# Kernel tuning notes

Hardware: AMD Instinct MI355X
Metric: run time of the kernel (lower is better)

The kernel has to match this reference:

```python
import jax, jax.numpy as jnp
import numpy as np

B, H, W = 8, 1024, 1024

SOBEL_X = jnp.array([[-1, 0, 1], [-2, 0, 2], [-1, 0, 1]], jnp.float32).reshape(1, 1, 3, 3)
SOBEL_Y = jnp.array([[-1, -2, -1], [0, 0, 0], [1, 2, 1]], jnp.float32).reshape(1, 1, 3, 3)
LAPLACIAN = jnp.array([[0, -1, 0], [-1, 4, -1], [0, -1, 0]], jnp.float32).reshape(1, 1, 3, 3)
TWO_PI = 2.0 * np.pi


def _conv(x, k, pad):
    return jax.lax.conv_general_dilated(
        x, k, window_strides=(1, 1), padding=[(pad, pad), (pad, pad)],
        dimension_numbers=('NCHW', 'OIHW', 'NCHW'))


def _boundary_mask(mask, w):
    ks = 2 * w + 1
    kernel = jnp.ones((1, 1, ks, ks), jnp.float32)
    s = _conv(mask, kernel, w)
    dilated = (s > 0).astype(jnp.float32)
    eroded = (s >= float(ks * ks)).astype(jnp.float32)
    return jnp.clip(dilated - eroded, 0.0, 1.0)


def _elev_grads(e):
    gx = _conv(e, SOBEL_X, 1)
    gy = _conv(e, SOBEL_Y, 1)
    mag = jnp.sqrt(gx * gx + gy * gy + 1e-8)
    dirn = jnp.arctan2(gy, gx + 1e-8)
    curv = _conv(e, LAPLACIAN, 1)
    return mag, dirn, curv


def _high_freq_mask(h, w):
    ii, jj = jnp.meshgrid(jnp.arange(h, dtype=jnp.float32), jnp.arange(w, dtype=jnp.float32), indexing='ij')
    dist = jnp.sqrt((ii - h // 2) ** 2 + (jj - w // 2) ** 2)
    return (dist > min(h, w) * 0.3).astype(jnp.float32).reshape(1, 1, h, w)


def setup_inputs() -> dict:
    key = jax.random.key(0)
    k1, k2, k3 = jax.random.split(key, 3)
    pred = jax.random.normal(k1, (B, 1, H, W), jnp.float32)
    target = jax.random.normal(k2, (B, 1, H, W), jnp.float32)
    mask = jax.random.randint(k3, (B, 1, H, W), 0, 2).astype(jnp.float32)
    return {'pred_elevation': pred, 'target_elevation': target, 'mask': mask}


def reference(pred_elevation, target_elevation, mask):
    # boundary masks for widths 1..3
    bms = [_boundary_mask(mask, w) for w in (1, 2, 3)]

    # ---- gradient continuity loss ----
    p_mag, p_dir, p_curv = _elev_grads(pred_elevation)
    t_mag, t_dir, t_curv = _elev_grads(target_elevation)
    slope_diff = jnp.abs(p_mag - t_mag)
    dir_diff = jnp.abs(p_dir - t_dir)
    dir_diff = jnp.minimum(dir_diff, TWO_PI - dir_diff)
    curv_diff = jnp.abs(p_curv - t_curv)
    grad_loss = 0.0
    for i, bm in enumerate(bms):
        w_sd = 1.0 if i == 0 else 0.5
        w_cv = 2.0 if i == 0 else 1.0
        grad_loss = grad_loss + w_sd * jnp.mean(slope_diff * bm)
        grad_loss = grad_loss + w_sd * jnp.mean(dir_diff * bm)
        grad_loss = grad_loss + w_cv * jnp.mean(curv_diff * bm)
    grad_loss = grad_loss / len(bms)

    # ---- frequency continuity loss ----
    pf = jnp.fft.fft2(pred_elevation)
    tf = jnp.fft.fft2(target_elevation)
    p_magf, t_magf = jnp.abs(pf), jnp.abs(tf)
    p_ph = jnp.arctan2(pf.imag, pf.real)
    t_ph = jnp.arctan2(tf.imag, tf.real)
    hf = _high_freq_mask(H, W)
    mag_loss = jnp.mean((p_magf * hf - t_magf * hf) ** 2)
    d = p_ph - t_ph
    phase_diff = jnp.arctan2(jnp.sin(d), jnp.cos(d))  # wrap to (-pi, pi]
    phase_loss = jnp.mean((phase_diff * hf) ** 2)
    freq_loss = mag_loss + 2.0 * phase_loss

    # ---- smoothness constraint (width_1 only) ----
    kern9 = jnp.ones((1, 1, 3, 3), jnp.float32) / 9.0
    local_mean = _conv(pred_elevation, kern9, 1)
    local_mean_sq = _conv(pred_elevation ** 2, kern9, 1)
    local_var = jnp.clip(local_mean_sq - local_mean ** 2, 1e-8, None)
    local_std = jnp.sqrt(local_var)
    smooth_loss = jnp.mean(local_std * bms[0])

    # ---- slope continuity (width_1 only) ----
    psx = _conv(p_mag, SOBEL_X, 1)
    psy = _conv(p_mag, SOBEL_Y, 1)
    p_change = jnp.sqrt(psx ** 2 + psy ** 2 + 1e-8)
    tsx = _conv(t_mag, SOBEL_X, 1)
    tsy = _conv(t_mag, SOBEL_Y, 1)
    t_change = jnp.sqrt(tsx ** 2 + tsy ** 2 + 1e-8)
    slope_loss = jnp.mean(jnp.abs(p_change - t_change) * bms[0])

    total = 2.0 * grad_loss + 1.5 * freq_loss + 3.0 * smooth_loss + 2.0 * slope_loss
    return (total, grad_loss, freq_loss, smooth_loss, slope_loss)
```

## Files before the change

### kernel.cpp

```cpp
#include <hip/hip_runtime.h>

#define HW 1024
#define TWO_PI_F 6.28318530717958647692f
#define NSLOT 64

__device__ __forceinline__ float2 cmulf(float2 a, float2 b){
  return make_float2(a.x*b.x - a.y*b.y, a.x*b.y + a.y*b.x);
}
__device__ __forceinline__ float fsqrt(float x){ return __builtin_amdgcn_sqrtf(x); }

__device__ __forceinline__ float fast_atan2_abs(float ay, float x){
  float ax = fabsf(x);
  float mx = fmaxf(ax, ay), mn = fminf(ax, ay);
  float a  = mn * __builtin_amdgcn_rcpf(fmaxf(mx, 1e-37f));
  float s  = a * a;
  float r  = ((((0.0208351f*s - 0.085133f)*s + 0.180141f)*s - 0.3302995f)*s
              + 0.999866f) * a;
  r = (ay > ax) ? 1.57079632679f - r : r;
  return (x < 0.f) ? 3.14159265359f - r : r;
}

__device__ __forceinline__ float block_reduce_add_f(float v, float* sc){
  int tid = threadIdx.x;
  #pragma unroll
  for (int o = 32; o > 0; o >>= 1) v += __shfl_down(v, o, 64);
  __syncthreads();
  if ((tid & 63) == 0) sc[tid >> 6] = v;
  __syncthreads();
  return sc[0] + sc[1] + sc[2] + sc[3];
}

__global__ void setup_kernel(double* acc, float2* twg){
  int i = threadIdx.x + blockIdx.x * 256;
  if (i < 5 * NSLOT) acc[i] = 0.0;
  if (i < 512){
    float s, c; sincosf(-TWO_PI_F * (float)i * (1.f/1024.f), &s, &c);
    twg[i] = make_float2(c, s);
  }
}

__global__ __launch_bounds__(256)
void spatial_kernel(const float* __restrict__ pred, const float* __restrict__ targ,
                    const float* __restrict__ mask, double* __restrict__ acc){
  __shared__ float sp[36*44];
  __shared__ float st[36*44];
  __shared__ float ov[2*34*35];
  __shared__ unsigned long long mrow[38];
  __shared__ float sc[4];
  float* const smkf = ov;
  float* const pmg  = ov;
  float* const tmg  = ov + 34*35;

  const int tid = threadIdx.x;
  const int x0 = blockIdx.x << 5, y0 = blockIdx.y << 5;
  const int z = blockIdx.z;
  const size_t ib = (size_t)z * ((size_t)HW * HW);
  const bool interior = ((unsigned)(blockIdx.x - 1) < 30u) &&
                        ((unsigned)(blockIdx.y - 1) < 30u);

  if (interior){
    const float* pb = pred + ib;
    const float* tb = targ + ib;
    for (int i = tid; i < 360; i += 256){
      int a = i / 10, b = i % 10;
      size_t off = (size_t)(y0 - 2 + a) * HW + (x0 - 4 + 4*b);
      float4 pv = *(const float4*)(pb + off);
      float4 tv = *(const float4*)(tb + off);
      int o = a*44 + 4*b;
      sp[o]=pv.x; sp[o+1]=pv.y; sp[o+2]=pv.z; sp[o+3]=pv.w;
      st[o]=tv.x; st[o+1]=tv.y; st[o+2]=tv.z; st[o+3]=tv.w;
    }
    const float* mb = mask + ib;
    for (int i = tid; i < 380; i += 256){
      int a = i / 10, b = i % 10;
      size_t off = (size_t)(y0 - 3 + a) * HW + (x0 - 4 + 4*b);
      float4 v = *(const float4*)(mb + off);
      int o = a*41 + 4*b;
      smkf[o]=v.x; smkf[o+1]=v.y; smkf[o+2]=v.z; smkf[o+3]=v.w;
    }
  } else {
    for (int i = tid; i < 1296; i += 256){
      int a = i / 36, b = i % 36;
      int gy = y0 - 2 + a, gx = x0 - 2 + b;
      float pv = 0.f, tv = 0.f;
      if ((unsigned)gy < HW && (unsigned)gx < HW){
        size_t idx = ib + (size_t)gy * HW + gx;
        pv = pred[idx]; tv = targ[idx];
      }
      sp[a*44 + b + 2] = pv; st[a*44 + b + 2] = tv;
    }
    for (int i = tid; i < 1444; i += 256){
      int a = i / 38, b = i % 38;
      int gy = y0 - 3 + a, gx = x0 - 3 + b;
      float v = 0.f;
      if ((unsigned)gy < HW && (unsigned)gx < HW) v = mask[ib + (size_t)gy * HW + gx];
      smkf[a*41 + b + 1] = v;
    }
  }
  __syncthreads();

  if (tid < 38){
    unsigned long long w = 0ull;
    #pragma unroll
    for (int x = 0; x < 38; x++)
      w |= (smkf[tid*41 + 1 + x] > 0.5f) ? (1ull << x) : 0ull;
    mrow[tid] = w;
  }
  __syncthreads();

  for (int i = tid; i < 1156; i += 256){
    int iy = i / 34, ix = i % 34;
    int gy = y0 - 1 + iy, gx = x0 - 1 + ix;
    float pv = 0.f, tv = 0.f;
    if ((unsigned)gy < HW && (unsigned)gx < HW){
      int o = iy*44 + ix + 2;
      float a00=sp[o], a01=sp[o+1], a02=sp[o+2];
      float a10=sp[o+44],           a12=sp[o+46];
      float a20=sp[o+88], a21=sp[o+89], a22=sp[o+90];
      float gxp = (a02 + 2.f*a12 + a22) - (a00 + 2.f*a10 + a20);
      float gyp = (a20 + 2.f*a21 + a22) - (a00 + 2.f*a01 + a02);
      pv = fsqrt(gxp*gxp + gyp*gyp + 1e-8f);
      float b00=st[o], b01=st[o+1], b02=st[o+2];
      float b10=st[o+44],           b12=st[o+46];
      float b20=st[o+88], b21=st[o+89], b22=st[o+90];
      float gxt = (b02 + 2.f*b12 + b22) - (b00 + 2.f*b10 + b20);
      float gyt = (b20 + 2.f*b21 + b22) - (b00 + 2.f*b01 + b02);
      tv = fsqrt(gxt*gxt + gyt*gyt + 1e-8f);
    }
    pmg[iy*35+ix] = pv; tmg[iy*35+ix] = tv;
  }
  __syncthreads();

  const int ty = tid >> 5, tx = tid & 31;
  const int r0 = ty << 2;

  int c1[10], c2[10], c3[10];
  #pragma unroll
  for (int j = 0; j < 10; j++){
    unsigned w = (unsigned)(mrow[r0 + j] >> tx);
    c3[j] = __popc(w & 0x7Fu);
    c2[j] = __popc((w >> 1) & 0x1Fu);
    c1[j] = __popc((w >> 2) & 0x7u);
  }

  float P[3][3], Q[3][3], A[3][3], B[3][3];
  #pragma unroll
  for (int rr = 0; rr < 3; rr++)
    #pragma unroll
    for (int cc = 0; cc < 3; cc++){
      P[rr][cc] = sp[(r0+1+rr)*44 + tx+3+cc];
      Q[rr][cc] = st[(r0+1+rr)*44 + tx+3+cc];
      A[rr][cc] = pmg[(r0+rr)*35 + tx+cc];
      B[rr][cc] = tmg[(r0+rr)*35 + tx+cc];
    }

  float accg = 0.f, accs = 0.f, accl = 0.f;
  #pragma unroll
  for (int k = 0; k < 4; k++){
    if (k){
      #pragma unroll
      for (int cc = 0; cc < 3; cc++){
        P[0][cc]=P[1][cc]; P[1][cc]=P[2][cc]; P[2][cc]=sp[(r0+k+3)*44 + tx+3+cc];
        Q[0][cc]=Q[1][cc]; Q[1][cc]=Q[2][cc]; Q[2][cc]=st[(r0+k+3)*44 + tx+3+cc];
        A[0][cc]=A[1][cc]; A[1][cc]=A[2][cc]; A[2][cc]=pmg[(r0+k+2)*35 + tx+cc];
        B[0][cc]=B[1][cc]; B[1][cc]=B[2][cc]; B[2][cc]=tmg[(r0+k+2)*35 + tx+cc];
      }
    }
    float gxp = (P[0][2]+2.f*P[1][2]+P[2][2]) - (P[0][0]+2.f*P[1][0]+P[2][0]);
    float gyp = (P[2][0]+2.f*P[2][1]+P[2][2]) - (P[0][0]+2.f*P[0][1]+P[0][2]);
    float cvp = 4.f*P[1][1] - P[0][1] - P[1][0] - P[1][2] - P[2][1];
    float gxt = (Q[0][2]+2.f*Q[1][2]+Q[2][2]) - (Q[0][0]+2.f*Q[1][0]+Q[2][0]);
    float gyt = (Q[2][0]+2.f*Q[2][1]+Q[2][2]) - (Q[0][0]+2.f*Q[0][1]+Q[0][2]);
    float cvt = 4.f*Q[1][1] - Q[0][1] - Q[1][0] - Q[1][2] - Q[2][1];

    float sd = fabsf(A[1][1] - B[1][1]);
    float x1 = gxp + 1e-8f, y1 = gyp;
    float x2 = gxt + 1e-8f, y2 = gyt;
    float dd = fast_atan2_abs(fabsf(y1*x2 - x1*y2), x1*x2 + y1*y2);
    float cd = fabsf(cvp - cvt);

    int s1 = c1[k+2]+c1[k+3]+c1[k+4];
    int s2 = c2[k+1]+c2[k+2]+c2[k+3]+c2[k+4]+c2[k+5];
    int s3 = c3[k]+c3[k+1]+c3[k+2]+c3[k+3]+c3[k+4]+c3[k+5]+c3[k+6];
    float w1 = ((unsigned)(s1 - 1) <  8u) ? 1.f : 0.f;
    float w2 = ((unsigned)(s2 - 1) < 24u) ? 1.f : 0.f;
    float w3 = ((unsigned)(s3 - 1) < 48u) ? 1.f : 0.f;

    accg += (sd + dd) * (w1 + 0.5f*(w2 + w3)) + cd * (2.f*w1 + w2 + w3);

    float s9 = 0.f, s9q = 0.f;
    #pragma unroll
    for (int rr = 0; rr < 3; rr++)
      #pragma unroll
      for (int cc = 0; cc < 3; cc++){ s9 += P[rr][cc]; s9q += P[rr][cc]*P[rr][cc]; }
    float lm = s9 * (1.f/9.f), lq = s9q * (1.f/9.f);
    accs += fsqrt(fmaxf(lq - lm*lm, 1e-8f)) * w1;

    float psx = (A[0][2]+2.f*A[1][2]+A[2][2]) - (A[0][0]+2.f*A[1][0]+A[2][0]);
    float psy = (A[2][0]+2.f*A[2][1]+A[2][2]) - (A[0][0]+2.f*A[0][1]+A[0][2]);
    float pch = fsqrt(psx*psx + psy*psy + 1e-8f);
    float tsx = (B[0][2]+2.f*B[1][2]+B[2][2]) - (B[0][0]+2.f*B[1][0]+B[2][0]);
    float tsy = (B[2][0]+2.f*B[2][1]+B[2][2]) - (B[0][0]+2.f*B[0][1]+B[0][2]);
    float tch = fsqrt(tsx*tsx + tsy*tsy + 1e-8f);
    accl += fabsf(pch - tch) * w1;
  }

  float g  = block_reduce_add_f(accg, sc);
  float sm = block_reduce_add_f(accs, sc);
  float sl = block_reduce_add_f(accl, sc);
  if (tid == 0){
    int slot = (blockIdx.x + blockIdx.y * 7 + z * 13) & (NSLOT - 1);
    atomicAdd(&acc[0*NSLOT + slot], (double)g);
    atomicAdd(&acc[1*NSLOT + slot], (double)sm);
    atomicAdd(&acc[2*NSLOT + slot], (double)sl);
  }
}

__device__ __forceinline__ float lane_xor(float x, int h, int lane){
  int xi = __float_as_int(x);
  int r;
  if (h == 1)       r = __builtin_amdgcn_update_dpp(xi, xi, 0xB1, 0xF, 0xF, true);
  else if (h == 2)  r = __builtin_amdgcn_update_dpp(xi, xi, 0x4E, 0xF, 0xF, true);
  else if (h == 8)  r = __builtin_amdgcn_update_dpp(xi, xi, 0x128, 0xF, 0xF, true);
  else if (h == 4)  r = __builtin_amdgcn_ds_swizzle(xi, 0x101F);
  else if (h == 16) r = __builtin_amdgcn_ds_swizzle(xi, 0x401F);
  else              r = __builtin_amdgcn_ds_bpermute((lane ^ 32) << 2, xi);
  return __int_as_float(r);
}

#define FC 0.70710678118654752f
#define FC1 0.92387953251128676f
#define FS1 0.38268343236508977f

__device__ __forceinline__ void bfly(float2& a, float2& b){
  float tx = b.x, ty = b.y;
  b.x = a.x - tx; b.y = a.y - ty;
  a.x += tx;      a.y += ty;
}
__device__ __forceinline__ void cmul_c(float2& b, float wr, float wi){
  float tx = wr*b.x - wi*b.y, ty = wr*b.y + wi*b.x;
  b.x = tx; b.y = ty;
}
__device__ __forceinline__ void rotmi(float2& b){
  float t = b.x; b.x = b.y; b.y = -t;
}

__device__ __forceinline__ void fft16_reg(float2* v){
  float2 y[16];
  y[0]=v[0];  y[1]=v[8];  y[2]=v[4];  y[3]=v[12];
  y[4]=v[2];  y[5]=v[10]; y[6]=v[6];  y[7]=v[14];
  y[8]=v[1];  y[9]=v[9];  y[10]=v[5]; y[11]=v[13];
  y[12]=v[3]; y[13]=v[11];y[14]=v[7]; y[15]=v[15];
  #pragma unroll
  for (int g = 0; g < 8; g++) bfly(y[2*g], y[2*g+1]);
  #pragma unroll
  for (int g = 0; g < 4; g++){
    int b = 4*g;
    bfly(y[b], y[b+2]);
    rotmi(y[b+3]); bfly(y[b+1], y[b+3]);
  }
  #pragma unroll
  for (int g = 0; g < 2; g++){
    int b = 8*g;
    bfly(y[b], y[b+4]);
    cmul_c(y[b+5],  FC, -FC); bfly(y[b+1], y[b+5]);
    rotmi(y[b+6]);            bfly(y[b+2], y[b+6]);
    cmul_c(y[b+7], -FC, -FC); bfly(y[b+3], y[b+7]);
  }
  bfly(y[0], y[8]);
  cmul_c(y[9],   FC1, -FS1); bfly(y[1], y[9]);
  cmul_c(y[10],  FC,  -FC);  bfly(y[2], y[10]);
  cmul_c(y[11],  FS1, -FC1); bfly(y[3], y[11]);
  rotmi(y[12]);              bfly(y[4], y[12]);
  cmul_c(y[13], -FS1, -FC1); bfly(y[5], y[13]);
  cmul_c(y[14], -FC,  -FC);  bfly(y[6], y[14]);
  cmul_c(y[15], -FC1, -FS1); bfly(y[7], y[15]);
  #pragma unroll
  for (int j = 0; j < 16; j++) v[j] = y[j];
}

__device__ __forceinline__ void fft1024_wave(float2* v, int lane,
                                             const float2* __restrict__ twg){
  {
    const float sgn = (lane & 1) ? -1.f : 1.f;
    #pragma unroll
    for (int j = 0; j < 16; j++){
      float ox = lane_xor(v[j].x, 1, lane);
      float oy = lane_xor(v[j].y, 1, lane);
      v[j].x = fmaf(sgn, v[j].x, ox);
      v[j].y = fmaf(sgn, v[j].y, oy);
    }
  }
  #pragma unroll
  for (int s = 1; s < 6; s++){
    const int h = 1 << s;
    const bool up = (lane & h) != 0;
    const float2 w = twg[(lane & (h - 1)) << (9 - s)];
    const float ewx = up ? w.x : 1.f;
    const float ewy = up ? w.y : 0.f;
    const float sgn = up ? -1.f : 1.f;
    #pragma unroll
    for (int j = 0; j < 16; j++){
      float tx = ewx*v[j].x - ewy*v[j].y;
      float ty = ewx*v[j].y + ewy*v[j].x;
      float ox = lane_xor(tx, h, lane);
      float oy = lane_xor(ty, h, lane);
      v[j].x = fmaf(sgn, tx, ox);
      v[j].y = fmaf(sgn, ty, oy);
    }
  }
  float2 w1 = twg[lane];
  float2 w2 = cmulf(w1, w1);
  float2 w3 = cmulf(w2, w1);
  float2 w4 = cmulf(w2, w2);
  float2 w5 = cmulf(w3, w2);
  float2 w6 = cmulf(w3, w3);
  float2 w7 = cmulf(w4, w3);
  float2 w8 = cmulf(w4, w4);
  v[1]  = cmulf(v[1],  w1);
  v[2]  = cmulf(v[2],  w2);
  v[3]  = cmulf(v[3],  w3);
  v[4]  = cmulf(v[4],  w4);
  v[5]  = cmulf(v[5],  w5);
  v[6]  = cmulf(v[6],  w6);
  v[7]  = cmulf(v[7],  w7);
  v[8]  = cmulf(v[8],  w8);
  v[9]  = cmulf(cmulf(v[9],  w8), w1);
  v[10] = cmulf(cmulf(v[10], w8), w2);
  v[11] = cmulf(cmulf(v[11], w8), w3);
  v[12] = cmulf(cmulf(v[12], w8), w4);
  v[13] = cmulf(cmulf(v[13], w8), w5);
  v[14] = cmulf(cmulf(v[14], w8), w6);
  v[15] = cmulf(cmulf(v[15], w8), w7);
  fft16_reg(v);
}

__global__ __launch_bounds__(512)
void fft_rows_t_kernel(const float* __restrict__ pred, const float* __restrict__ targ,
                       float2* __restrict__ Zt, const float2* __restrict__ twg){
  __shared__ float2 tile[8][64][9];
  const int tid = threadIdx.x;
  const int lane = tid & 63;
  const int w = tid >> 6;
  const int y0 = blockIdx.x << 3;
  const size_t ibase = ((size_t)blockIdx.y * HW + (y0 + w)) * HW;
  const int rb = __brev(lane) >> 26;
  const float4* p4 = (const float4*)(pred + ibase);
  const float4* t4 = (const float4*)(targ + ibase);
  float2 v[16];
  #pragma unroll
  for (int m = 0; m < 4; m++){
    float4 a = p4[4*rb + m];
    float4 b = t4[4*rb + m];
    v[4*m+0] = make_float2(a.x, b.x);
    v[4*m+1] = make_float2(a.y, b.y);
    v[4*m+2] = make_float2(a.z, b.z);
    v[4*m+3] = make_float2(a.w, b.w);
  }
  fft1024_wave(v, lane, twg);
  float2* zb = Zt + (size_t)blockIdx.y * HW * HW + (size_t)blockIdx.x * 8192;
  const int yl = tid & 7, kl = tid >> 3;
  #pragma unroll
  for (int jb = 0; jb < 2; jb++){
    __syncthreads();
    #pragma unroll
    for (int jj = 0; jj < 8; jj++) tile[jj][lane][w] = v[8*jb + jj];
    __syncthreads();
    #pragma unroll
    for (int jj = 0; jj < 8; jj++){
      int k = ((jb << 3) + jj) * 64 + kl;
      zb[k * 8 + yl] = tile[jj][kl][yl];
    }
  }
}

__device__ __forceinline__ void freq_contrib(float2 Zk, float2 Zm, int k1, int k2,
                                             float& ms, float& ps){
  int di = k1 - 512, dj = k2 - 512;
  if (di*di + dj*dj < 94372) return;
  float pr = 0.5f*(Zk.x + Zm.x);
  float pi = 0.5f*(Zk.y - Zm.y);
  float tr = 0.5f*(Zk.y + Zm.y);
  float ti = 0.5f*(Zm.x - Zk.x);
  float p2 = pr*pr + pi*pi;
  float t2 = tr*tr + ti*ti;
  ms += p2 + t2 - 2.f*fsqrt(p2*t2);
  float re = pr*tr + pi*ti;
  float im = pi*tr - pr*ti;
  float pd = fast_atan2_abs(fabsf(im), re);
  ps += pd*pd;
}

__global__ __launch_bounds__(256)
void fft_cols2_kernel(const float2* __restrict__ Z, const float2* __restrict__ twg,
                      double* __restrict__ acc){
  __shared__ float2 ex[4][1024];
  const int lane = threadIdx.x & 63;
  const int w = threadIdx.x >> 6;
  const int p = 2 * blockIdx.x + (w >> 1);
  const bool valid = (p <= 512);
  const int r = (w & 1) ? ((1024 - p) & 1023) : p;
  const float2* base = Z + (size_t)blockIdx.y * HW * HW;
  const int rb = __brev(lane) >> 26;

  float2 v[16];
  if (valid){
    const float4* f4 = (const float4*)base;
    #pragma unroll
    for (int s = 0; s < 2; s++){
      size_t o = (size_t)(2*rb + s) * 4096 + (size_t)r * 4;
      #pragma unroll
      for (int q = 0; q < 4; q++){
        float4 x = f4[o + q];
        v[8*s + 2*q]     = make_float2(x.x, x.y);
        v[8*s + 2*q + 1] = make_float2(x.z, x.w);
      }
    }
    fft1024_wave(v, lane, twg);
    #pragma unroll
    for (int j = 0; j < 16; j++) ex[w][lane + (j << 6)] = v[j];
  }
  __syncthreads();
  if (!valid) return;
  const bool self = (p == 0) || (p == 512);
  if ((w & 1) && self) return;

  const float2* pb = ex[w ^ 1];
  float ms = 0.f, ps = 0.f;
  #pragma unroll
  for (int j = 0; j < 16; j++){
    int k = lane + (j << 6);
    float2 zm = pb[(1024 - k) & 1023];
    freq_contrib(v[j], zm, k, r, ms, ps);
  }
  #pragma unroll
  for (int o = 32; o > 0; o >>= 1){
    ms += __shfl_down(ms, o, 64);
    ps += __shfl_down(ps, o, 64);
  }
  if (lane == 0){
    int slot = (r + blockIdx.y * 11) & (NSLOT - 1);
    atomicAdd(&acc[3*NSLOT + slot], (double)ms);
    atomicAdd(&acc[4*NSLOT + slot], (double)ps);
  }
}

__global__ void finalize_kernel(const double* __restrict__ acc, float* __restrict__ out){
  const int t = threadIdx.x;
  double v[5];
  #pragma unroll
  for (int s = 0; s < 5; s++) v[s] = acc[s*NSLOT + t];
  #pragma unroll
  for (int o = 32; o > 0; o >>= 1)
    #pragma unroll
    for (int s = 0; s < 5; s++) v[s] += __shfl_down(v[s], o, 64);
  if (t == 0){
    const double inv = 1.0 / 8388608.0;
    double grad   = v[0] * inv / 3.0;
    double smooth = v[1] * inv;
    double slope  = v[2] * inv;
    double freq   = (v[3] + 2.0 * v[4]) * inv;
    double total  = 2.0*grad + 1.5*freq + 3.0*smooth + 2.0*slope;
    out[0] = (float)total;
    out[1] = (float)grad;
    out[2] = (float)freq;
    out[3] = (float)smooth;
    out[4] = (float)slope;
  }
}

extern "C" void kernel_launch(void* const* d_in, const int* in_sizes, int n_in,
                              void* d_out, int out_size, void* d_ws, size_t ws_size,
                              hipStream_t stream){
  const float* pred = (const float*)d_in[0];
  const float* targ = (const float*)d_in[1];
  const float* mask = (const float*)d_in[2];
  double* acc  = (double*)d_ws;
  float2* twg  = (float2*)((char*)d_ws + 4096);
  float2* Z    = (float2*)((char*)d_ws + 8192);

  setup_kernel<<<2, 256, 0, stream>>>(acc, twg);
  spatial_kernel<<<dim3(32, 32, 8), 256, 0, stream>>>(pred, targ, mask, acc);
  fft_rows_t_kernel<<<dim3(128, 8), 512, 0, stream>>>(pred, targ, Z, twg);
  fft_cols2_kernel<<<dim3(257, 8), 256, 0, stream>>>(Z, twg, acc);
  finalize_kernel<<<1, 64, 0, stream>>>(acc, (float*)d_out);
}
```

Measured before the change: 236.6 us.

## Interleave pred/target in shared memory as float2 and pack popcount windows

Stores pred and target interleaved as 2-wide vectors in LDS so each stencil load fetches both, and the Sobel arithmetic can use packed FP32 ops. It also splits the magnitude pass into interior and border branches, packs three popcount counters into one int so the window sums share additions, adds an occupancy hint to launch bounds, and replaces the cross-half bpermute in the FFT with permlane32_swap. These target LDS instruction count, ALU work and register pressure in the spatial kernel, at the risk of different bank-conflict behaviour from the 8-byte stride.

```diff
diff --git a/kernel.cpp b/kernel.cpp
--- a/kernel.cpp
+++ b/kernel.cpp
@@ -3,6 +3,12 @@
 #define HW 1024
 #define TWO_PI_F 6.28318530717958647692f
 #define NSLOT 64
+
+typedef float v2f __attribute__((ext_vector_type(2)));
+typedef int   i2v __attribute__((ext_vector_type(2)));
+
+__device__ __forceinline__ v2f mkv2(float a, float b){ v2f r; r.x = a; r.y = b; return r; }
+__device__ __forceinline__ v2f v2s(float s){ v2f r; r.x = s; r.y = s; return r; }
 
 __device__ __forceinline__ float2 cmulf(float2 a, float2 b){
   return make_float2(a.x*b.x - a.y*b.y, a.x*b.y + a.y*b.x);
@@ -39,17 +45,14 @@
   }
 }
 
-__global__ __launch_bounds__(256)
+__global__ __launch_bounds__(256, 4)
 void spatial_kernel(const float* __restrict__ pred, const float* __restrict__ targ,
                     const float* __restrict__ mask, double* __restrict__ acc){
-  __shared__ float sp[36*44];
-  __shared__ float st[36*44];
-  __shared__ float ov[2*34*35];
+  __shared__ v2f spt[36*44];
+  __shared__ v2f pmt[34*35];
   __shared__ unsigned long long mrow[38];
   __shared__ float sc[4];
-  float* const smkf = ov;
-  float* const pmg  = ov;
-  float* const tmg  = ov + 34*35;
+  float* const smkf = (float*)pmt;
 
   const int tid = threadIdx.x;
   const int x0 = blockIdx.x << 5, y0 = blockIdx.y << 5;
@@ -67,8 +70,10 @@
       float4 pv = *(const float4*)(pb + off);
       float4 tv = *(const float4*)(tb + off);
       int o = a*44 + 4*b;
-      sp[o]=pv.x; sp[o+1]=pv.y; sp[o+2]=pv.z; sp[o+3]=pv.w;
-      st[o]=tv.x; st[o+1]=tv.y; st[o+2]=tv.z; st[o+3]=tv.w;
+      spt[o+0] = mkv2(pv.x, tv.x);
+      spt[o+1] = mkv2(pv.y, tv.y);
+      spt[o+2] = mkv2(pv.z, tv.z);
+      spt[o+3] = mkv2(pv.w, tv.w);
     }
     const float* mb = mask + ib;
     for (int i = tid; i < 380; i += 256){
@@ -87,7 +92,7 @@
         size_t idx = ib + (size_t)gy * HW + gx;
         pv = pred[idx]; tv = targ[idx];
       }
-      sp[a*44 + b + 2] = pv; st[a*44 + b + 2] = tv;
+      spt[a*44 + b + 2] = mkv2(pv, tv);
     }
     for (int i = tid; i < 1444; i += 256){
       int a = i / 38, b = i % 38;
@@ -99,59 +104,67 @@
   }
   __syncthreads();
 
+  unsigned long long mw = 0ull;
   if (tid < 38){
-    unsigned long long w = 0ull;
     #pragma unroll
     for (int x = 0; x < 38; x++)
-      w |= (smkf[tid*41 + 1 + x] > 0.5f) ? (1ull << x) : 0ull;
-    mrow[tid] = w;
-  }
-  __syncthreads();
-
-  for (int i = tid; i < 1156; i += 256){
-    int iy = i / 34, ix = i % 34;
-    int gy = y0 - 1 + iy, gx = x0 - 1 + ix;
-    float pv = 0.f, tv = 0.f;
-    if ((unsigned)gy < HW && (unsigned)gx < HW){
+      mw |= (smkf[tid*41 + 1 + x] > 0.5f) ? (1ull << x) : 0ull;
+  }
+  __syncthreads();
+  if (tid < 38) mrow[tid] = mw;
+
+  if (interior){
+    for (int i = tid; i < 1156; i += 256){
+      int iy = i / 34, ix = i % 34;
       int o = iy*44 + ix + 2;
-      float a00=sp[o], a01=sp[o+1], a02=sp[o+2];
-      float a10=sp[o+44],           a12=sp[o+46];
-      float a20=sp[o+88], a21=sp[o+89], a22=sp[o+90];
-      float gxp = (a02 + 2.f*a12 + a22) - (a00 + 2.f*a10 + a20);
-      float gyp = (a20 + 2.f*a21 + a22) - (a00 + 2.f*a01 + a02);
-      pv = fsqrt(gxp*gxp + gyp*gyp + 1e-8f);
-      float b00=st[o], b01=st[o+1], b02=st[o+2];
-      float b10=st[o+44],           b12=st[o+46];
-      float b20=st[o+88], b21=st[o+89], b22=st[o+90];
-      float gxt = (b02 + 2.f*b12 + b22) - (b00 + 2.f*b10 + b20);
-      float gyt = (b20 + 2.f*b21 + b22) - (b00 + 2.f*b01 + b02);
-      tv = fsqrt(gxt*gxt + gyt*gyt + 1e-8f);
-    }
-    pmg[iy*35+ix] = pv; tmg[iy*35+ix] = tv;
+      v2f a00=spt[o],    a01=spt[o+1],  a02=spt[o+2];
+      v2f a10=spt[o+44],                a12=spt[o+46];
+      v2f a20=spt[o+88], a21=spt[o+89], a22=spt[o+90];
+      v2f gx = (a02 + v2s(2.f)*a12 + a22) - (a00 + v2s(2.f)*a10 + a20);
+      v2f gy = (a20 + v2s(2.f)*a21 + a22) - (a00 + v2s(2.f)*a01 + a02);
+      v2f m2 = gx*gx + gy*gy + v2s(1e-8f);
+      pmt[iy*35+ix] = mkv2(fsqrt(m2.x), fsqrt(m2.y));
+    }
+  } else {
+    for (int i = tid; i < 1156; i += 256){
+      int iy = i / 34, ix = i % 34;
+      int gy = y0 - 1 + iy, gx = x0 - 1 + ix;
+      v2f out = v2s(0.f);
+      if ((unsigned)gy < HW && (unsigned)gx < HW){
+        int o = iy*44 + ix + 2;
+        v2f a00=spt[o],    a01=spt[o+1],  a02=spt[o+2];
+        v2f a10=spt[o+44],                a12=spt[o+46];
+        v2f a20=spt[o+88], a21=spt[o+89], a22=spt[o+90];
+        v2f gxv = (a02 + v2s(2.f)*a12 + a22) - (a00 + v2s(2.f)*a10 + a20);
+        v2f gyv = (a20 + v2s(2.f)*a21 + a22) - (a00 + v2s(2.f)*a01 + a02);
+        v2f m2 = gxv*gxv + gyv*gyv + v2s(1e-8f);
+        out = mkv2(fsqrt(m2.x), fsqrt(m2.y));
+      }
+      pmt[iy*35+ix] = out;
+    }
   }
   __syncthreads();
 
   const int ty = tid >> 5, tx = tid & 31;
   const int r0 = ty << 2;
 
-  int c1[10], c2[10], c3[10];
+  int cp[10];
   #pragma unroll
   for (int j = 0; j < 10; j++){
     unsigned w = (unsigned)(mrow[r0 + j] >> tx);
-    c3[j] = __popc(w & 0x7Fu);
-    c2[j] = __popc((w >> 1) & 0x1Fu);
-    c1[j] = __popc((w >> 2) & 0x7u);
-  }
-
-  float P[3][3], Q[3][3], A[3][3], B[3][3];
+    int c3 = __popc(w & 0x7Fu);
+    int c2 = __popc((w >> 1) & 0x1Fu);
+    int c1 = __popc((w >> 2) & 0x7u);
+    cp[j] = c1 | (c2 << 8) | (c3 << 16);
+  }
+
+  v2f PQ[3][3], AB[3][3];
   #pragma unroll
   for (int rr = 0; rr < 3; rr++)
     #pragma unroll
     for (int cc = 0; cc < 3; cc++){
-      P[rr][cc] = sp[(r0+1+rr)*44 + tx+3+cc];
-      Q[rr][cc] = st[(r0+1+rr)*44 + tx+3+cc];
-      A[rr][cc] = pmg[(r0+rr)*35 + tx+cc];
-      B[rr][cc] = tmg[(r0+rr)*35 + tx+cc];
+      PQ[rr][cc] = spt[(r0+1+rr)*44 + tx+3+cc];
+      AB[rr][cc] = pmt[(r0+rr)*35 + tx+cc];
     }
 
   float accg = 0.f, accs = 0.f, accl = 0.f;
@@ -160,28 +173,26 @@
     if (k){
       #pragma unroll
       for (int cc = 0; cc < 3; cc++){
-        P[0][cc]=P[1][cc]; P[1][cc]=P[2][cc]; P[2][cc]=sp[(r0+k+3)*44 + tx+3+cc];
-        Q[0][cc]=Q[1][cc]; Q[1][cc]=Q[2][cc]; Q[2][cc]=st[(r0+k+3)*44 + tx+3+cc];
-        A[0][cc]=A[1][cc]; A[1][cc]=A[2][cc]; A[2][cc]=pmg[(r0+k+2)*35 + tx+cc];
-        B[0][cc]=B[1][cc]; B[1][cc]=B[2][cc]; B[2][cc]=tmg[(r0+k+2)*35 + tx+cc];
+        PQ[0][cc]=PQ[1][cc]; PQ[1][cc]=PQ[2][cc]; PQ[2][cc]=spt[(r0+k+3)*44 + tx+3+cc];
+        AB[0][cc]=AB[1][cc]; AB[1][cc]=AB[2][cc]; AB[2][cc]=pmt[(r0+k+2)*35 + tx+cc];
       }
     }
-    float gxp = (P[0][2]+2.f*P[1][2]+P[2][2]) - (P[0][0]+2.f*P[1][0]+P[2][0]);
-    float gyp = (P[2][0]+2.f*P[2][1]+P[2][2]) - (P[0][0]+2.f*P[0][1]+P[0][2]);
-    float cvp = 4.f*P[1][1] - P[0][1] - P[1][0] - P[1][2] - P[2][1];
-    float gxt = (Q[0][2]+2.f*Q[1][2]+Q[2][2]) - (Q[0][0]+2.f*Q[1][0]+Q[2][0]);
-    float gyt = (Q[2][0]+2.f*Q[2][1]+Q[2][2]) - (Q[0][0]+2.f*Q[0][1]+Q[0][2]);
-    float cvt = 4.f*Q[1][1] - Q[0][1] - Q[1][0] - Q[1][2] - Q[2][1];
-
-    float sd = fabsf(A[1][1] - B[1][1]);
-    float x1 = gxp + 1e-8f, y1 = gyp;
-    float x2 = gxt + 1e-8f, y2 = gyt;
+    v2f gxv = (PQ[0][2] + v2s(2.f)*PQ[1][2] + PQ[2][2]) - (PQ[0][0] + v2s(2.f)*PQ[1][0] + PQ[2][0]);
+    v2f gyv = (PQ[2][0] + v2s(2.f)*PQ[2][1] + PQ[2][2]) - (PQ[0][0] + v2s(2.f)*PQ[0][1] + PQ[0][2]);
+    v2f cvv = v2s(4.f)*PQ[1][1] - PQ[0][1] - PQ[1][0] - PQ[1][2] - PQ[2][1];
+
+    float sd = fabsf(AB[1][1].x - AB[1][1].y);
+    float x1 = gxv.x + 1e-8f, y1 = gyv.x;
+    float x2 = gxv.y + 1e-8f, y2 = gyv.y;
     float dd = fast_atan2_abs(fabsf(y1*x2 - x1*y2), x1*x2 + y1*y2);
-    float cd = fabsf(cvp - cvt);
-
-    int s1 = c1[k+2]+c1[k+3]+c1[k+4];
-    int s2 = c2[k+1]+c2[k+2]+c2[k+3]+c2[k+4]+c2[k+5];
-    int s3 = c3[k]+c3[k+1]+c3[k+2]+c3[k+3]+c3[k+4]+c3[k+5]+c3[k+6];
+    float cd = fabsf(cvv.x - cvv.y);
+
+    int s1p = cp[k+2] + cp[k+3] + cp[k+4];
+    int s2p = s1p + cp[k+1] + cp[k+5];
+    int s3p = s2p + cp[k]   + cp[k+6];
+    int s1 = s1p & 0xFF;
+    int s2 = (s2p >> 8) & 0xFF;
+    int s3 = s3p >> 16;
     float w1 = ((unsigned)(s1 - 1) <  8u) ? 1.f : 0.f;
     float w2 = ((unsigned)(s2 - 1) < 24u) ? 1.f : 0.f;
     float w3 = ((unsigned)(s3 - 1) < 48u) ? 1.f : 0.f;
@@ -192,17 +203,14 @@
     #pragma unroll
     for (int rr = 0; rr < 3; rr++)
       #pragma unroll
-      for (int cc = 0; cc < 3; cc++){ s9 += P[rr][cc]; s9q += P[rr][cc]*P[rr][cc]; }
+      for (int cc = 0; cc < 3; cc++){ float p = PQ[rr][cc].x; s9 += p; s9q += p*p; }
     float lm = s9 * (1.f/9.f), lq = s9q * (1.f/9.f);
     accs += fsqrt(fmaxf(lq - lm*lm, 1e-8f)) * w1;
 
-    float psx = (A[0][2]+2.f*A[1][2]+A[2][2]) - (A[0][0]+2.f*A[1][0]+A[2][0]);
-    float psy = (A[2][0]+2.f*A[2][1]+A[2][2]) - (A[0][0]+2.f*A[0][1]+A[0][2]);
-    float pch = fsqrt(psx*psx + psy*psy + 1e-8f);
-    float tsx = (B[0][2]+2.f*B[1][2]+B[2][2]) - (B[0][0]+2.f*B[1][0]+B[2][0]);
-    float tsy = (B[2][0]+2.f*B[2][1]+B[2][2]) - (B[0][0]+2.f*B[0][1]+B[0][2]);
-    float tch = fsqrt(tsx*tsx + tsy*tsy + 1e-8f);
-    accl += fabsf(pch - tch) * w1;
+    v2f px = (AB[0][2] + v2s(2.f)*AB[1][2] + AB[2][2]) - (AB[0][0] + v2s(2.f)*AB[1][0] + AB[2][0]);
+    v2f py = (AB[2][0] + v2s(2.f)*AB[2][1] + AB[2][2]) - (AB[0][0] + v2s(2.f)*AB[0][1] + AB[0][2]);
+    v2f ch2 = px*px + py*py + v2s(1e-8f);
+    accl += fabsf(fsqrt(ch2.x) - fsqrt(ch2.y)) * w1;
   }
 
   float g  = block_reduce_add_f(accg, sc);
@@ -224,7 +232,10 @@
   else if (h == 8)  r = __builtin_amdgcn_update_dpp(xi, xi, 0x128, 0xF, 0xF, true);
   else if (h == 4)  r = __builtin_amdgcn_ds_swizzle(xi, 0x101F);
   else if (h == 16) r = __builtin_amdgcn_ds_swizzle(xi, 0x401F);
-  else              r = __builtin_amdgcn_ds_bpermute((lane ^ 32) << 2, xi);
+  else {
+    i2v pr = __builtin_amdgcn_permlane32_swap(xi, xi, false, false);
+    r = (lane & 32) ? pr.x : pr.y;
+  }
   return __int_as_float(r);
 }
 
```

Result: faster. 227.4 us (-3.9%).
